# Optimization experiments

Measured on AMD Instinct MI355X. Metric: run time of the kernel, lower is better.

## Reference

```python
import jax, jax.numpy as jnp
import numpy as np

B_, CIN, HH, WW = 2, 64, 64, 64
D_MODEL, D_INNER, D_STATE, DT_RANK, D_CONV = 64, 128, 16, 32, 3


def setup_inputs() -> dict:
    key = jax.random.key(0)
    ks = jax.random.split(key, 16)
    w = lambda k, shape: jax.random.normal(k, shape, jnp.float32) * 0.05
    # dt_proj bias init (torch: inv-softplus of dt sampled in [dt_min, dt_max])
    dt = jnp.exp(jax.random.uniform(ks[10], (D_INNER,)) * (np.log(0.1) - np.log(0.001)) + np.log(0.001))
    dt = jnp.clip(dt, 1e-4, None)
    inv_dt = dt + jnp.log(-jnp.expm1(-dt))
    A = jnp.tile(jnp.arange(1, D_STATE + 1, dtype=jnp.float32), (D_INNER, 1))
    return {
        "rgb_feat": jax.random.normal(ks[0], (B_, CIN, HH, WW), jnp.float32),
        "dte_feat": jax.random.normal(ks[1], (B_, CIN, HH, WW), jnp.float32),
        "conv1_w": w(ks[2], (D_MODEL, CIN)), "conv1_b": jnp.zeros((D_MODEL,), jnp.float32),
        "conv2_w": w(ks[3], (D_MODEL, CIN)), "conv2_b": jnp.zeros((D_MODEL,), jnp.float32),
        "conv3_w": w(ks[4], (CIN, D_MODEL)), "conv3_b": jnp.zeros((CIN,), jnp.float32),
        "norm_w": jnp.ones((D_MODEL,), jnp.float32),
        "in_proj_w": w(ks[5], (2 * D_INNER, D_MODEL)),
        "conv1d_w": w(ks[6], (D_INNER, D_CONV)), "conv1d_b": jnp.zeros((D_INNER,), jnp.float32),
        "x_proj_w": w(ks[7], (DT_RANK + 2 * D_STATE, D_INNER)),
        "dt_proj_w": jax.random.uniform(ks[8], (D_INNER, DT_RANK), jnp.float32, -DT_RANK ** -0.5, DT_RANK ** -0.5),
        "dt_proj_b": inv_dt,
        "A_log": jnp.log(A),
        "Dp": jnp.ones((D_INNER,), jnp.float32),
        "out_proj_w": w(ks[9], (D_MODEL, D_INNER)),
    }


def _conv1x1(x, w, b):
    return jnp.einsum('bchw,oc->bohw', x, w) + b[None, :, None, None]


def _rmsnorm(x, w, eps=1e-5):
    return x * jax.lax.rsqrt(jnp.mean(x * x, axis=-1, keepdims=True) + eps) * w


def _dwconv1d(x, w, b):
    # x: [B,L,D]; depthwise conv, kernel 3, padding 1 (same length)
    xt = jnp.transpose(x, (0, 2, 1))  # [B,D,L]
    y = jax.lax.conv_general_dilated(xt, w[:, None, :], (1,), [(1, 1)],
                                     dimension_numbers=('NCH', 'OIH', 'NCH'),
                                     feature_group_count=D_INNER)
    return jnp.transpose(y + b[None, :, None], (0, 2, 1))


def _mamba(x, h, p):
    # x: [B,L,d_model]
    xz = x @ p['in_proj_w'].T                      # [B,L,2*d_inner]
    xc, z = jnp.split(xz, 2, axis=-1)
    xc = jax.nn.silu(_dwconv1d(xc, p['conv1d_w'], p['conv1d_b']))
    A = -jnp.exp(p['A_log'])                       # [D,S]
    dbc = xc @ p['x_proj_w'].T                     # [B,L,dt_rank+2S]
    delta, Bm, Cm = jnp.split(dbc, [DT_RANK, DT_RANK + D_STATE], axis=-1)
    delta = jax.nn.softplus(delta @ p['dt_proj_w'].T + p['dt_proj_b'])  # [B,L,D]
    deltaA = jnp.exp(delta[..., None] * A)         # [B,L,D,S]
    BX = delta[..., None] * Bm[:, :, None, :] * xc[..., None]  # [B,L,D,S]
    h = deltaA * h + BX
    y = jnp.einsum('blds,bls->bld', h, Cm) + p['Dp'] * xc
    out = (y * jax.nn.silu(z)) @ p['out_proj_w'].T
    return out, h


def _residual_block(x4d, h, p):
    B, C, H, W = x4d.shape
    x = jnp.transpose(x4d.reshape(B, C, H * W), (0, 2, 1))  # [B,L,C]
    x = _rmsnorm(x, p['norm_w'])
    out, h = _mamba(x, h, p)
    out = out + x
    return jnp.transpose(out, (0, 2, 1)).reshape(B, C, H, W), h


def _rsfm(rgb_feat, dte_feat, conv1_w, conv1_b, conv2_w, conv2_b, conv3_w, conv3_b,
          norm_w, in_proj_w, conv1d_w, conv1d_b, x_proj_w, dt_proj_w, dt_proj_b,
          A_log, Dp, out_proj_w):
    p = dict(norm_w=norm_w, in_proj_w=in_proj_w, conv1d_w=conv1d_w, conv1d_b=conv1d_b,
             x_proj_w=x_proj_w, dt_proj_w=dt_proj_w, dt_proj_b=dt_proj_b,
             A_log=A_log, Dp=Dp, out_proj_w=out_proj_w)
    rgb = _conv1x1(rgb_feat, conv1_w, conv1_b)
    dte = _conv1x1(dte_feat, conv2_w, conv2_b)
    B = rgb.shape[0]
    h = jnp.zeros((B, HH * WW, D_INNER, D_STATE), jnp.float32)
    out1, h = _residual_block(rgb, h, p)
    out2, h = _residual_block(dte + out1, h, p)
    out3, h = _residual_block(rgb + out2, h, p)
    out4, h = _residual_block(dte + out3, h, p)
    out5, h = _residual_block(rgb + out4, h, p)
    out6, h = _residual_block(dte + out5, h, p)
    return _conv1x1(out6, conv3_w, conv3_b), h


def reference(rgb_feat, dte_feat, conv1_w, conv1_b, conv2_w, conv2_b, conv3_w, conv3_b,
              norm_w, in_proj_w, conv1d_w, conv1d_b, x_proj_w, dt_proj_w, dt_proj_b,
              A_log, Dp, out_proj_w):
    return _rsfm(rgb_feat, dte_feat, conv1_w, conv1_b, conv2_w, conv2_b, conv3_w, conv3_b,
                 norm_w, in_proj_w, conv1d_w, conv1d_b, x_proj_w, dt_proj_w, dt_proj_b,
                 A_log, Dp, out_proj_w)
```

## Files before the change

### kernel.cpp

```cpp
#include <hip/hip_runtime.h>

typedef unsigned short u16;
typedef unsigned int u32;

#define LSEQ 4096
#define NPOS 8192

__device__ __forceinline__ float bf2f(u16 u){
  union { u32 i; float f; } v; v.i = ((u32)u) << 16; return v.f;
}
__device__ __forceinline__ u16 f2bf(float f){
  union { float f; u32 i; } v; v.f = f;
  u32 x = v.i;
  return (u16)((x + 0x7fffu + ((x >> 16) & 1u)) >> 16);
}
__device__ __forceinline__ float2 up2(u32 u){
  union { u32 i; float f; } a, b;
  a.i = u << 16; b.i = u & 0xffff0000u;
  float2 r; r.x = a.f; r.y = b.f; return r;
}
__device__ __forceinline__ u32 pk2(float a, float b){
  return (u32)f2bf(a) | ((u32)f2bf(b) << 16);
}
__device__ __forceinline__ float silu_f(float x){ return x / (1.f + __expf(-x)); }
__device__ __forceinline__ float softplus_f(float x){
  return fmaxf(x, 0.f) + log1pf(__expf(-fabsf(x)));
}

__global__ __launch_bounds__(256) void k_prep(
    const float* __restrict__ ipw, const float* __restrict__ xpw,
    const float* __restrict__ dtw, const float* __restrict__ opw,
    const float* __restrict__ w1, const float* __restrict__ w2,
    const float* __restrict__ w3, const float* __restrict__ alog,
    float* __restrict__ ipT, float* __restrict__ xpT,
    float* __restrict__ dtT, float* __restrict__ opT,
    float* __restrict__ w1T, float* __restrict__ w2T,
    float* __restrict__ w3T, float* __restrict__ Aneg)
{
  int t = blockIdx.x * 256 + threadIdx.x;
  if (t < 16384){ int o = t >> 6, c = t & 63; ipT[c * 256 + o] = ipw[t]; }
  if (t < 8192){ int o = t >> 7, d = t & 127; xpT[d * 64 + o] = xpw[t]; }
  if (t < 4096){ int d = t >> 5, r = t & 31; dtT[r * 128 + d] = dtw[t]; }
  if (t < 8192){ int o = t >> 7, d = t & 127; opT[d * 64 + o] = opw[t]; }
  if (t < 4096){ int o = t >> 6, c = t & 63;
                 w1T[c*64+o] = w1[t]; w2T[c*64+o] = w2[t]; w3T[c*64+o] = w3[t]; }
  if (t < 2048){ Aneg[t] = -__expf(alog[t]); }
}

__global__ __launch_bounds__(256) void k_convin(
    const float* __restrict__ rgb, const float* __restrict__ dte,
    const float* __restrict__ w1T, const float* __restrict__ b1,
    const float* __restrict__ w2T, const float* __restrict__ b2,
    float* __restrict__ rgbp, float* __restrict__ dtep)
{
  __shared__ __align__(16) float xt[64][64];
  __shared__ __align__(16) float ot[64][65];
  const int tid = threadIdx.x;
  const int which = blockIdx.x & 1;
  const int n0 = (blockIdx.x >> 1) * 64;
  const int b = n0 >> 12, l0 = n0 & 4095;
  const float* src = which ? dte : rgb;
  const float* wT  = which ? w2T : w1T;
  const float* bb  = which ? b2 : b1;
  float* o = which ? dtep : rgbp;

  #pragma unroll
  for (int j = 0; j < 16; j++){
    int idx = tid + 256 * j;
    int c = idx >> 6, p = idx & 63;
    xt[c][p] = src[(size_t)b * 262144 + (size_t)c * 4096 + l0 + p];
  }
  __syncthreads();

  const int pos = tid & 63;
  const int cb  = (tid >> 6) * 16;
  float acc[16];
  #pragma unroll
  for (int j = 0; j < 16; j++) acc[j] = bb[cb + j];
  for (int c = 0; c < 64; c++){
    float xv = xt[c][pos];
    #pragma unroll
    for (int j = 0; j < 16; j++) acc[j] += wT[c*64 + cb + j] * xv;
  }
  #pragma unroll
  for (int j = 0; j < 16; j++) ot[pos][cb + j] = acc[j];
  __syncthreads();
  #pragma unroll
  for (int j = 0; j < 16; j++){
    int idx = tid + 256 * j;
    int p = idx >> 6, c = idx & 63;
    o[(size_t)(n0 + p)*64 + c] = ot[p][c];
  }
}

__global__ __launch_bounds__(256) void k_pre(
    const float* __restrict__ xin, const float* __restrict__ normw,
    const float* __restrict__ ipT,
    float* __restrict__ xn, float* __restrict__ xcp, float* __restrict__ zs)
{
  __shared__ __align__(16) float xnl[4][2][64];
  const int wv = threadIdx.x >> 6, lane = threadIdx.x & 63;
  const int n0 = (blockIdx.x * 4 + wv) * 2;
  float nw = normw[lane];
  #pragma unroll
  for (int p = 0; p < 2; p++){
    int n = n0 + p;
    float v = xin[(size_t)n*64 + lane];
    float ss = v * v;
    for (int m = 32; m > 0; m >>= 1) ss += __shfl_xor(ss, m);
    v = v * rsqrtf(ss * (1.f/64.f) + 1e-5f) * nw;
    xn[(size_t)n*64 + lane] = v;
    xnl[wv][p][lane] = v;
  }
  float ac[2][4] = {};
  for (int c = 0; c < 64; c++){
    float w0 = ipT[c*256 + lane],       w1 = ipT[c*256 + 64 + lane];
    float w2 = ipT[c*256 + 128 + lane], w3 = ipT[c*256 + 192 + lane];
    #pragma unroll
    for (int p = 0; p < 2; p++){
      float xv = xnl[wv][p][c];
      ac[p][0] += w0*xv; ac[p][1] += w1*xv; ac[p][2] += w2*xv; ac[p][3] += w3*xv;
    }
  }
  #pragma unroll
  for (int p = 0; p < 2; p++){
    int n = n0 + p;
    xcp[(size_t)n*128 + lane]      = ac[p][0];
    xcp[(size_t)n*128 + 64 + lane] = ac[p][1];
    zs[(size_t)n*128 + lane]       = silu_f(ac[p][2]);
    zs[(size_t)n*128 + 64 + lane]  = silu_f(ac[p][3]);
  }
}

__global__ __launch_bounds__(256) void k_step(
    const float* __restrict__ xcpA, float* __restrict__ xcpB,
    float* __restrict__ zs, float* __restrict__ xn,
    u16* __restrict__ hbf, float* __restrict__ hfin,
    const float* __restrict__ base_next,
    const float* __restrict__ xpT, const float* __restrict__ dtT,
    const float* __restrict__ opT, const float* __restrict__ Aneg,
    const float* __restrict__ c1w, const float* __restrict__ c1b,
    const float* __restrict__ dtb, const float* __restrict__ Dpw,
    const float* __restrict__ normw, const float* __restrict__ ipT,
    int hasH, int fusePre)
{
  __shared__ __align__(16) float xcl[4][2][128];
  __shared__ __align__(16) float dbl[4][2][64];
  __shared__ __align__(16) float yzl[4][2][128];
  __shared__ __align__(16) float xnl[4][2][64];
  const int wv = threadIdx.x >> 6, lane = threadIdx.x & 63;
  const int n0 = (blockIdx.x * 4 + wv) * 2;
  const int d0 = lane, d1 = 64 + lane;

  float cw00 = c1w[d0*3+0], cw01 = c1w[d0*3+1], cw02 = c1w[d0*3+2];
  float cw10 = c1w[d1*3+0], cw11 = c1w[d1*3+1], cw12 = c1w[d1*3+2];
  float cb0 = c1b[d0], cb1 = c1b[d1];

  float xc0[2], xc1[2];
  #pragma unroll
  for (int p = 0; p < 2; p++){
    int n = n0 + p, l = n & 4095;
    const float* xr = xcpA + (size_t)n * 128;
    float am0 = 0.f, am1 = 0.f, ap0 = 0.f, ap1 = 0.f;
    if (l > 0)    { am0 = xr[d0 - 128]; am1 = xr[d1 - 128]; }
    float a00 = xr[d0], a01 = xr[d1];
    if (l < 4095) { ap0 = xr[d0 + 128]; ap1 = xr[d1 + 128]; }
    float v0 = silu_f(cw00*am0 + cw01*a00 + cw02*ap0 + cb0);
    float v1 = silu_f(cw10*am1 + cw11*a01 + cw12*ap1 + cb1);
    xc0[p] = v0; xc1[p] = v1;
    xcl[wv][p][d0] = v0; xcl[wv][p][d1] = v1;
  }

  {
    float xa[2] = {0,0};
    for (int d = 0; d < 128; d++){
      float w = xpT[d*64 + lane];
      #pragma unroll
      for (int p = 0; p < 2; p++) xa[p] += w * xcl[wv][p][d];
    }
    #pragma unroll
    for (int p = 0; p < 2; p++) dbl[wv][p][lane] = xa[p];
  }

  float dl0[2], dl1[2];
  {
    float tb0 = dtb[d0], tb1 = dtb[d1];
    float da0[2] = {tb0, tb0}, da1[2] = {tb1, tb1};
    for (int r = 0; r < 32; r++){
      float w0 = dtT[r*128 + d0], w1 = dtT[r*128 + d1];
      #pragma unroll
      for (int p = 0; p < 2; p++){
        float bv = dbl[wv][p][r];
        da0[p] += w0 * bv; da1[p] += w1 * bv;
      }
    }
    #pragma unroll
    for (int p = 0; p < 2; p++){ dl0[p] = softplus_f(da0[p]); dl1[p] = softplus_f(da1[p]); }
  }

  float an0[16], an1[16];
  {
    const float4* A0 = (const float4*)(Aneg + d0*16);
    const float4* A1 = (const float4*)(Aneg + d1*16);
    #pragma unroll
    for (int q = 0; q < 4; q++){
      float4 a = A0[q]; an0[q*4+0]=a.x; an0[q*4+1]=a.y; an0[q*4+2]=a.z; an0[q*4+3]=a.w;
      float4 b = A1[q]; an1[q*4+0]=b.x; an1[q*4+1]=b.y; an1[q*4+2]=b.z; an1[q*4+3]=b.w;
    }
  }
  float dp0 = Dpw[d0], dp1 = Dpw[d1];

  #pragma unroll 1
  for (int p = 0; p < 2; p++){
    int n = n0 + p;
    float Bm[16], Cm[16];
    {
      const float4* bb = (const float4*)&dbl[wv][p][32];
      const float4* cc = (const float4*)&dbl[wv][p][48];
      #pragma unroll
      for (int q = 0; q < 4; q++){
        float4 a = bb[q]; Bm[q*4+0]=a.x; Bm[q*4+1]=a.y; Bm[q*4+2]=a.z; Bm[q*4+3]=a.w;
        float4 b = cc[q]; Cm[q*4+0]=b.x; Cm[q*4+1]=b.y; Cm[q*4+2]=b.z; Cm[q*4+3]=b.w;
      }
    }
    u16* hp0 = hbf + ((size_t)n*2048 + (size_t)d0*16);
    u16* hp1 = hbf + ((size_t)n*2048 + (size_t)d1*16);
    float h0[16], h1[16];
    if (hasH){
      #pragma unroll
      for (int q = 0; q < 2; q++){
        uint4 v = ((const uint4*)hp0)[q];
        float2 t0=up2(v.x), t1=up2(v.y), t2=up2(v.z), t3=up2(v.w);
        h0[q*8+0]=t0.x; h0[q*8+1]=t0.y; h0[q*8+2]=t1.x; h0[q*8+3]=t1.y;
        h0[q*8+4]=t2.x; h0[q*8+5]=t2.y; h0[q*8+6]=t3.x; h0[q*8+7]=t3.y;
        uint4 w = ((const uint4*)hp1)[q];
        float2 s0=up2(w.x), s1=up2(w.y), s2=up2(w.z), s3=up2(w.w);
        h1[q*8+0]=s0.x; h1[q*8+1]=s0.y; h1[q*8+2]=s1.x; h1[q*8+3]=s1.y;
        h1[q*8+4]=s2.x; h1[q*8+5]=s2.y; h1[q*8+6]=s3.x; h1[q*8+7]=s3.y;
      }
    } else {
      #pragma unroll
      for (int s = 0; s < 16; s++){ h0[s]=0.f; h1[s]=0.f; }
    }
    float y0 = 0.f, y1 = 0.f;
    float bx0 = dl0[p] * xc0[p], bx1 = dl1[p] * xc1[p];
    #pragma unroll
    for (int s = 0; s < 16; s++){
      h0[s] = __expf(dl0[p]*an0[s])*h0[s] + bx0*Bm[s];
      y0 = fmaf(h0[s], Cm[s], y0);
      h1[s] = __expf(dl1[p]*an1[s])*h1[s] + bx1*Bm[s];
      y1 = fmaf(h1[s], Cm[s], y1);
    }
    if (fusePre){
      #pragma unroll
      for (int q = 0; q < 2; q++){
        uint4 v;
        v.x = pk2(h0[q*8+0], h0[q*8+1]); v.y = pk2(h0[q*8+2], h0[q*8+3]);
        v.z = pk2(h0[q*8+4], h0[q*8+5]); v.w = pk2(h0[q*8+6], h0[q*8+7]);
        ((uint4*)hp0)[q] = v;
        uint4 w;
        w.x = pk2(h1[q*8+0], h1[q*8+1]); w.y = pk2(h1[q*8+2], h1[q*8+3]);
        w.z = pk2(h1[q*8+4], h1[q*8+5]); w.w = pk2(h1[q*8+6], h1[q*8+7]);
        ((uint4*)hp1)[q] = w;
      }
    } else {
      float4* f0 = (float4*)(hfin + (size_t)n*2048 + (size_t)d0*16);
      float4* f1 = (float4*)(hfin + (size_t)n*2048 + (size_t)d1*16);
      #pragma unroll
      for (int q = 0; q < 4; q++){
        float4 v; v.x=h0[q*4+0]; v.y=h0[q*4+1]; v.z=h0[q*4+2]; v.w=h0[q*4+3];
        f0[q] = v;
        float4 w; w.x=h1[q*4+0]; w.y=h1[q*4+1]; w.z=h1[q*4+2]; w.w=h1[q*4+3];
        f1[q] = w;
      }
    }
    y0 += dp0 * xc0[p];
    y1 += dp1 * xc1[p];
    yzl[wv][p][d0] = y0 * zs[(size_t)n*128 + d0];
    yzl[wv][p][d1] = y1 * zs[(size_t)n*128 + d1];
  }

  float oa[2] = {0,0};
  for (int d = 0; d < 128; d++){
    float w = opT[d*64 + lane];
    #pragma unroll
    for (int p = 0; p < 2; p++) oa[p] += w * yzl[wv][p][d];
  }

  float nw = normw[lane];
  if (fusePre){
    #pragma unroll
    for (int p = 0; p < 2; p++){
      int n = n0 + p;
      float v = oa[p] + xn[(size_t)n*64 + lane] + base_next[(size_t)n*64 + lane];
      float ss = v * v;
      for (int m = 32; m > 0; m >>= 1) ss += __shfl_xor(ss, m);
      v = v * rsqrtf(ss * (1.f/64.f) + 1e-5f) * nw;
      xn[(size_t)n*64 + lane] = v;
      xnl[wv][p][lane] = v;
    }
    float ac[2][4] = {};
    for (int c = 0; c < 64; c++){
      float w0 = ipT[c*256 + lane],       w1 = ipT[c*256 + 64 + lane];
      float w2 = ipT[c*256 + 128 + lane], w3 = ipT[c*256 + 192 + lane];
      #pragma unroll
      for (int p = 0; p < 2; p++){
        float xv = xnl[wv][p][c];
        ac[p][0] += w0*xv; ac[p][1] += w1*xv; ac[p][2] += w2*xv; ac[p][3] += w3*xv;
      }
    }
    #pragma unroll
    for (int p = 0; p < 2; p++){
      int n = n0 + p;
      xcpB[(size_t)n*128 + lane]      = ac[p][0];
      xcpB[(size_t)n*128 + 64 + lane] = ac[p][1];
      zs[(size_t)n*128 + lane]        = silu_f(ac[p][2]);
      zs[(size_t)n*128 + 64 + lane]   = silu_f(ac[p][3]);
    }
  } else {
    #pragma unroll
    for (int p = 0; p < 2; p++){
      int n = n0 + p;
      xcpB[(size_t)n*64 + lane] = oa[p] + xn[(size_t)n*64 + lane];
    }
  }
}

__global__ __launch_bounds__(256) void k_conv3(
    const float* __restrict__ out6, const float* __restrict__ w3T,
    const float* __restrict__ b3, float* __restrict__ out)
{
  __shared__ __align__(16) float t[64][65];
  const int tid = threadIdx.x;
  const int n0 = blockIdx.x * 64;
  #pragma unroll
  for (int i = 0; i < 16; i++){
    int idx = tid + 256*i;
    int r = idx >> 6, c = idx & 63;
    t[r][c] = out6[(size_t)(n0 + r)*64 + c];
  }
  __syncthreads();
  const int i = tid & 63;
  const int cb = (tid >> 6) * 16;
  float acc[16];
  #pragma unroll
  for (int j = 0; j < 16; j++) acc[j] = b3[cb + j];
  for (int o = 0; o < 64; o++){
    float xv = t[i][o];
    #pragma unroll
    for (int j = 0; j < 16; j++) acc[j] += w3T[o*64 + cb + j] * xv;
  }
  const int b = n0 >> 12;
  const int l = (n0 & 4095) + i;
  #pragma unroll
  for (int j = 0; j < 16; j++)
    out[(size_t)b*262144 + (size_t)(cb + j)*4096 + l] = acc[j];
}

extern "C" void kernel_launch(void* const* d_in, const int* in_sizes, int n_in,
                              void* d_out, int out_size, void* d_ws, size_t ws_size,
                              hipStream_t stream)
{
  const float* rgb  = (const float*)d_in[0];
  const float* dte  = (const float*)d_in[1];
  const float* w1   = (const float*)d_in[2];
  const float* b1   = (const float*)d_in[3];
  const float* w2   = (const float*)d_in[4];
  const float* b2   = (const float*)d_in[5];
  const float* w3   = (const float*)d_in[6];
  const float* b3   = (const float*)d_in[7];
  const float* nrm  = (const float*)d_in[8];
  const float* ipw  = (const float*)d_in[9];
  const float* c1w  = (const float*)d_in[10];
  const float* c1b  = (const float*)d_in[11];
  const float* xpw  = (const float*)d_in[12];
  const float* dtw  = (const float*)d_in[13];
  const float* dtb  = (const float*)d_in[14];
  const float* alog = (const float*)d_in[15];
  const float* Dpw  = (const float*)d_in[16];
  const float* opw  = (const float*)d_in[17];

  float* outc = (float*)d_out;
  float* hfin = outc + 524288;

  float* ws   = (float*)d_ws;
  float* xcp0 = ws;
  float* xcp1 = ws + 1048576;
  float* rgbp = ws + 2097152;
  float* dtep = ws + 2621440;
  float* xnb  = ws + 3145728;
  float* zsb  = ws + 3670016;
  float* wb   = ws + 4718592;
  float* ipT  = wb;
  float* xpT  = wb + 16384;
  float* dtT  = wb + 24576;
  float* opT  = wb + 28672;
  float* w1T  = wb + 36864;
  float* w2T  = wb + 40960;
  float* w3T  = wb + 45056;
  float* Aneg = wb + 49152;
  u16*   hbf  = (u16*)(ws + 4769792);

  k_prep<<<64, 256, 0, stream>>>(ipw, xpw, dtw, opw, w1, w2, w3, alog,
                                 ipT, xpT, dtT, opT, w1T, w2T, w3T, Aneg);
  k_convin<<<256, 256, 0, stream>>>(rgb, dte, w1T, b1, w2T, b2, rgbp, dtep);
  k_pre<<<1024, 256, 0, stream>>>(rgbp, nrm, ipT, xnb, xcp0, zsb);

  float* xa[2] = {xcp0, xcp1};
  for (int k = 0; k < 6; k++){
    const float* base = (k == 5) ? rgbp  : ((k & 1) ? rgbp : dtep);
    k_step<<<1024, 256, 0, stream>>>(xa[k & 1], xa[(k & 1) ^ 1], zsb, xnb,
                                     hbf, hfin, base,
                                     xpT, dtT, opT, Aneg, c1w, c1b, dtb, Dpw,
                                     nrm, ipT, (k > 0) ? 1 : 0, (k < 5) ? 1 : 0);
  }
  k_conv3<<<128, 256, 0, stream>>>(xcp0, w3T, b3, outc);
}
```

Baseline: 369.5 us.

## Fuse all residual blocks into one kernel with halo-recompute tiles

Replaces the chain of conv-in, pre, six step kernels and conv-out with a single kernel. Each block handles 32 positions plus an 8-position halo on each side, and recomputes the halo so the depthwise conv stays local across all six blocks. The bf16 SSM state lives in registers and activations stay in shared memory, which removes the per-step global round trips of state and activations. The cost is redundant halo compute (48 positions computed per 32 output), higher register and LDS pressure, and only 256 blocks to fill the GPU.

```diff
diff --git a/kernel.cpp b/kernel.cpp
--- a/kernel.cpp
+++ b/kernel.cpp
@@ -3,21 +3,15 @@
 typedef unsigned short u16;
 typedef unsigned int u32;
 
-#define LSEQ 4096
-#define NPOS 8192
-
-__device__ __forceinline__ float bf2f(u16 u){
-  union { u32 i; float f; } v; v.i = ((u32)u) << 16; return v.f;
+__device__ __forceinline__ float2 up2(u32 u){
+  union { u32 i; float f; } a, b;
+  a.i = u << 16; b.i = u & 0xffff0000u;
+  float2 r; r.x = a.f; r.y = b.f; return r;
 }
 __device__ __forceinline__ u16 f2bf(float f){
   union { float f; u32 i; } v; v.f = f;
   u32 x = v.i;
   return (u16)((x + 0x7fffu + ((x >> 16) & 1u)) >> 16);
-}
-__device__ __forceinline__ float2 up2(u32 u){
-  union { u32 i; float f; } a, b;
-  a.i = u << 16; b.i = u & 0xffff0000u;
-  float2 r; r.x = a.f; r.y = b.f; return r;
 }
 __device__ __forceinline__ u32 pk2(float a, float b){
   return (u32)f2bf(a) | ((u32)f2bf(b) << 16);
@@ -47,314 +41,300 @@
   if (t < 2048){ Aneg[t] = -__expf(alog[t]); }
 }
 
-__global__ __launch_bounds__(256) void k_convin(
+#define CPB 48
+#define PPW 6
+
+__global__ __launch_bounds__(512, 2) void k_fused(
     const float* __restrict__ rgb, const float* __restrict__ dte,
     const float* __restrict__ w1T, const float* __restrict__ b1,
     const float* __restrict__ w2T, const float* __restrict__ b2,
-    float* __restrict__ rgbp, float* __restrict__ dtep)
-{
-  __shared__ __align__(16) float xt[64][64];
-  __shared__ __align__(16) float ot[64][65];
-  const int tid = threadIdx.x;
-  const int which = blockIdx.x & 1;
-  const int n0 = (blockIdx.x >> 1) * 64;
-  const int b = n0 >> 12, l0 = n0 & 4095;
-  const float* src = which ? dte : rgb;
-  const float* wT  = which ? w2T : w1T;
-  const float* bb  = which ? b2 : b1;
-  float* o = which ? dtep : rgbp;
-
-  #pragma unroll
-  for (int j = 0; j < 16; j++){
-    int idx = tid + 256 * j;
-    int c = idx >> 6, p = idx & 63;
-    xt[c][p] = src[(size_t)b * 262144 + (size_t)c * 4096 + l0 + p];
-  }
-  __syncthreads();
-
-  const int pos = tid & 63;
-  const int cb  = (tid >> 6) * 16;
-  float acc[16];
-  #pragma unroll
-  for (int j = 0; j < 16; j++) acc[j] = bb[cb + j];
-  for (int c = 0; c < 64; c++){
-    float xv = xt[c][pos];
-    #pragma unroll
-    for (int j = 0; j < 16; j++) acc[j] += wT[c*64 + cb + j] * xv;
-  }
-  #pragma unroll
-  for (int j = 0; j < 16; j++) ot[pos][cb + j] = acc[j];
-  __syncthreads();
-  #pragma unroll
-  for (int j = 0; j < 16; j++){
-    int idx = tid + 256 * j;
-    int p = idx >> 6, c = idx & 63;
-    o[(size_t)(n0 + p)*64 + c] = ot[p][c];
-  }
-}
-
-__global__ __launch_bounds__(256) void k_pre(
-    const float* __restrict__ xin, const float* __restrict__ normw,
-    const float* __restrict__ ipT,
-    float* __restrict__ xn, float* __restrict__ xcp, float* __restrict__ zs)
-{
-  __shared__ __align__(16) float xnl[4][2][64];
-  const int wv = threadIdx.x >> 6, lane = threadIdx.x & 63;
-  const int n0 = (blockIdx.x * 4 + wv) * 2;
-  float nw = normw[lane];
-  #pragma unroll
-  for (int p = 0; p < 2; p++){
-    int n = n0 + p;
-    float v = xin[(size_t)n*64 + lane];
-    float ss = v * v;
-    for (int m = 32; m > 0; m >>= 1) ss += __shfl_xor(ss, m);
-    v = v * rsqrtf(ss * (1.f/64.f) + 1e-5f) * nw;
-    xn[(size_t)n*64 + lane] = v;
-    xnl[wv][p][lane] = v;
-  }
-  float ac[2][4] = {};
-  for (int c = 0; c < 64; c++){
-    float w0 = ipT[c*256 + lane],       w1 = ipT[c*256 + 64 + lane];
-    float w2 = ipT[c*256 + 128 + lane], w3 = ipT[c*256 + 192 + lane];
-    #pragma unroll
-    for (int p = 0; p < 2; p++){
-      float xv = xnl[wv][p][c];
-      ac[p][0] += w0*xv; ac[p][1] += w1*xv; ac[p][2] += w2*xv; ac[p][3] += w3*xv;
-    }
-  }
-  #pragma unroll
-  for (int p = 0; p < 2; p++){
-    int n = n0 + p;
-    xcp[(size_t)n*128 + lane]      = ac[p][0];
-    xcp[(size_t)n*128 + 64 + lane] = ac[p][1];
-    zs[(size_t)n*128 + lane]       = silu_f(ac[p][2]);
-    zs[(size_t)n*128 + 64 + lane]  = silu_f(ac[p][3]);
-  }
-}
-
-__global__ __launch_bounds__(256) void k_step(
-    const float* __restrict__ xcpA, float* __restrict__ xcpB,
-    float* __restrict__ zs, float* __restrict__ xn,
-    u16* __restrict__ hbf, float* __restrict__ hfin,
-    const float* __restrict__ base_next,
+    const float* __restrict__ w3T, const float* __restrict__ b3,
+    const float* __restrict__ normw, const float* __restrict__ ipT,
     const float* __restrict__ xpT, const float* __restrict__ dtT,
     const float* __restrict__ opT, const float* __restrict__ Aneg,
     const float* __restrict__ c1w, const float* __restrict__ c1b,
     const float* __restrict__ dtb, const float* __restrict__ Dpw,
-    const float* __restrict__ normw, const float* __restrict__ ipT,
-    int hasH, int fusePre)
+    float* __restrict__ outc, float* __restrict__ hfin)
 {
-  __shared__ __align__(16) float xcl[4][2][128];
-  __shared__ __align__(16) float dbl[4][2][64];
-  __shared__ __align__(16) float yzl[4][2][128];
-  __shared__ __align__(16) float xnl[4][2][64];
-  const int wv = threadIdx.x >> 6, lane = threadIdx.x & 63;
-  const int n0 = (blockIdx.x * 4 + wv) * 2;
+  __shared__ __align__(16) float xcp[CPB][128];
+  __shared__ __align__(16) float xcs[CPB][128];
+  __shared__ __align__(16) float dblS[CPB][64];
+  __shared__ __align__(16) float xns[CPB][64];
+  __shared__ __align__(16) float bA[CPB][64];
+  __shared__ __align__(16) float bB[CPB][64];
+  __shared__ __align__(16) float ansS[16][129];
+  __shared__ __align__(16) float xpW[8192];
+  __shared__ __align__(16) float dtW[4096];
+
+  const int tid = threadIdx.x;
+  const int wv = tid >> 6, lane = tid & 63;
+  const int b = blockIdx.x;
+  const int batch = b >> 7;
+  const int lbase = ((b & 127) << 5) - 8;
+  const int cpw = wv * PPW;
   const int d0 = lane, d1 = 64 + lane;
 
-  float cw00 = c1w[d0*3+0], cw01 = c1w[d0*3+1], cw02 = c1w[d0*3+2];
-  float cw10 = c1w[d1*3+0], cw11 = c1w[d1*3+1], cw12 = c1w[d1*3+2];
-  float cb0 = c1b[d0], cb1 = c1b[d1];
-
-  float xc0[2], xc1[2];
+  for (int i = tid; i < 8192; i += 512) xpW[i] = xpT[i];
+  for (int i = tid; i < 4096; i += 512) dtW[i] = dtT[i];
+  for (int i = tid; i < 2048; i += 512) ansS[i & 15][i >> 4] = Aneg[i];
+
+  const float cw00 = c1w[d0*3+0], cw01 = c1w[d0*3+1], cw02 = c1w[d0*3+2];
+  const float cw10 = c1w[d1*3+0], cw11 = c1w[d1*3+1], cw12 = c1w[d1*3+2];
+  const float cb0 = c1b[d0], cb1 = c1b[d1];
+  const float tb0 = dtb[d0], tb1 = dtb[d1];
+  const float dp0 = Dpw[d0], dp1 = Dpw[d1];
+  const float nw = normw[lane];
+
+  int lp[PPW];
   #pragma unroll
-  for (int p = 0; p < 2; p++){
-    int n = n0 + p, l = n & 4095;
-    const float* xr = xcpA + (size_t)n * 128;
-    float am0 = 0.f, am1 = 0.f, ap0 = 0.f, ap1 = 0.f;
-    if (l > 0)    { am0 = xr[d0 - 128]; am1 = xr[d1 - 128]; }
-    float a00 = xr[d0], a01 = xr[d1];
-    if (l < 4095) { ap0 = xr[d0 + 128]; ap1 = xr[d1 + 128]; }
-    float v0 = silu_f(cw00*am0 + cw01*a00 + cw02*ap0 + cb0);
-    float v1 = silu_f(cw10*am1 + cw11*a01 + cw12*ap1 + cb1);
-    xc0[p] = v0; xc1[p] = v1;
-    xcl[wv][p][d0] = v0; xcl[wv][p][d1] = v1;
+  for (int p = 0; p < PPW; p++) lp[p] = lbase + cpw + p;
+
+  {
+    const float* rp = rgb + (size_t)batch * 262144;
+    const float* dq_ = dte + (size_t)batch * 262144;
+    int lc[PPW];
+    #pragma unroll
+    for (int p = 0; p < PPW; p++) lc[p] = min(max(lp[p], 0), 4095);
+    float accA[PPW], accB[PPW];
+    float bb1 = b1[lane], bb2 = b2[lane];
+    #pragma unroll
+    for (int p = 0; p < PPW; p++){ accA[p] = bb1; accB[p] = bb2; }
+    #pragma unroll 4
+    for (int c = 0; c < 64; c++){
+      float wA = w1T[c*64 + lane], wB = w2T[c*64 + lane];
+      const float* rc = rp + c*4096;
+      const float* dc = dq_ + c*4096;
+      #pragma unroll
+      for (int p = 0; p < PPW; p++){
+        accA[p] = fmaf(wA, rc[lc[p]], accA[p]);
+        accB[p] = fmaf(wB, dc[lc[p]], accB[p]);
+      }
+    }
+    #pragma unroll
+    for (int p = 0; p < PPW; p++){ bA[cpw+p][lane] = accA[p]; bB[cpw+p][lane] = accB[p]; }
   }
 
+  float xnr[PPW], zs0[PPW], zs1[PPW];
   {
-    float xa[2] = {0,0};
-    for (int d = 0; d < 128; d++){
-      float w = xpT[d*64 + lane];
-      #pragma unroll
-      for (int p = 0; p < 2; p++) xa[p] += w * xcl[wv][p][d];
-    }
-    #pragma unroll
-    for (int p = 0; p < 2; p++) dbl[wv][p][lane] = xa[p];
-  }
-
-  float dl0[2], dl1[2];
-  {
-    float tb0 = dtb[d0], tb1 = dtb[d1];
-    float da0[2] = {tb0, tb0}, da1[2] = {tb1, tb1};
-    for (int r = 0; r < 32; r++){
-      float w0 = dtT[r*128 + d0], w1 = dtT[r*128 + d1];
-      #pragma unroll
-      for (int p = 0; p < 2; p++){
-        float bv = dbl[wv][p][r];
-        da0[p] += w0 * bv; da1[p] += w1 * bv;
-      }
-    }
-    #pragma unroll
-    for (int p = 0; p < 2; p++){ dl0[p] = softplus_f(da0[p]); dl1[p] = softplus_f(da1[p]); }
-  }
-
-  float an0[16], an1[16];
-  {
-    const float4* A0 = (const float4*)(Aneg + d0*16);
-    const float4* A1 = (const float4*)(Aneg + d1*16);
-    #pragma unroll
-    for (int q = 0; q < 4; q++){
-      float4 a = A0[q]; an0[q*4+0]=a.x; an0[q*4+1]=a.y; an0[q*4+2]=a.z; an0[q*4+3]=a.w;
-      float4 b = A1[q]; an1[q*4+0]=b.x; an1[q*4+1]=b.y; an1[q*4+2]=b.z; an1[q*4+3]=b.w;
-    }
-  }
-  float dp0 = Dpw[d0], dp1 = Dpw[d1];
-
-  #pragma unroll 1
-  for (int p = 0; p < 2; p++){
-    int n = n0 + p;
-    float Bm[16], Cm[16];
-    {
-      const float4* bb = (const float4*)&dbl[wv][p][32];
-      const float4* cc = (const float4*)&dbl[wv][p][48];
-      #pragma unroll
-      for (int q = 0; q < 4; q++){
-        float4 a = bb[q]; Bm[q*4+0]=a.x; Bm[q*4+1]=a.y; Bm[q*4+2]=a.z; Bm[q*4+3]=a.w;
-        float4 b = cc[q]; Cm[q*4+0]=b.x; Cm[q*4+1]=b.y; Cm[q*4+2]=b.z; Cm[q*4+3]=b.w;
-      }
-    }
-    u16* hp0 = hbf + ((size_t)n*2048 + (size_t)d0*16);
-    u16* hp1 = hbf + ((size_t)n*2048 + (size_t)d1*16);
-    float h0[16], h1[16];
-    if (hasH){
-      #pragma unroll
-      for (int q = 0; q < 2; q++){
-        uint4 v = ((const uint4*)hp0)[q];
-        float2 t0=up2(v.x), t1=up2(v.y), t2=up2(v.z), t3=up2(v.w);
-        h0[q*8+0]=t0.x; h0[q*8+1]=t0.y; h0[q*8+2]=t1.x; h0[q*8+3]=t1.y;
-        h0[q*8+4]=t2.x; h0[q*8+5]=t2.y; h0[q*8+6]=t3.x; h0[q*8+7]=t3.y;
-        uint4 w = ((const uint4*)hp1)[q];
-        float2 s0=up2(w.x), s1=up2(w.y), s2=up2(w.z), s3=up2(w.w);
-        h1[q*8+0]=s0.x; h1[q*8+1]=s0.y; h1[q*8+2]=s1.x; h1[q*8+3]=s1.y;
-        h1[q*8+4]=s2.x; h1[q*8+5]=s2.y; h1[q*8+6]=s3.x; h1[q*8+7]=s3.y;
-      }
-    } else {
-      #pragma unroll
-      for (int s = 0; s < 16; s++){ h0[s]=0.f; h1[s]=0.f; }
-    }
-    float y0 = 0.f, y1 = 0.f;
-    float bx0 = dl0[p] * xc0[p], bx1 = dl1[p] * xc1[p];
-    #pragma unroll
-    for (int s = 0; s < 16; s++){
-      h0[s] = __expf(dl0[p]*an0[s])*h0[s] + bx0*Bm[s];
-      y0 = fmaf(h0[s], Cm[s], y0);
-      h1[s] = __expf(dl1[p]*an1[s])*h1[s] + bx1*Bm[s];
-      y1 = fmaf(h1[s], Cm[s], y1);
-    }
-    if (fusePre){
-      #pragma unroll
-      for (int q = 0; q < 2; q++){
-        uint4 v;
-        v.x = pk2(h0[q*8+0], h0[q*8+1]); v.y = pk2(h0[q*8+2], h0[q*8+3]);
-        v.z = pk2(h0[q*8+4], h0[q*8+5]); v.w = pk2(h0[q*8+6], h0[q*8+7]);
-        ((uint4*)hp0)[q] = v;
-        uint4 w;
-        w.x = pk2(h1[q*8+0], h1[q*8+1]); w.y = pk2(h1[q*8+2], h1[q*8+3]);
-        w.z = pk2(h1[q*8+4], h1[q*8+5]); w.w = pk2(h1[q*8+6], h1[q*8+7]);
-        ((uint4*)hp1)[q] = w;
-      }
-    } else {
-      float4* f0 = (float4*)(hfin + (size_t)n*2048 + (size_t)d0*16);
-      float4* f1 = (float4*)(hfin + (size_t)n*2048 + (size_t)d1*16);
-      #pragma unroll
-      for (int q = 0; q < 4; q++){
-        float4 v; v.x=h0[q*4+0]; v.y=h0[q*4+1]; v.z=h0[q*4+2]; v.w=h0[q*4+3];
-        f0[q] = v;
-        float4 w; w.x=h1[q*4+0]; w.y=h1[q*4+1]; w.z=h1[q*4+2]; w.w=h1[q*4+3];
-        f1[q] = w;
-      }
-    }
-    y0 += dp0 * xc0[p];
-    y1 += dp1 * xc1[p];
-    yzl[wv][p][d0] = y0 * zs[(size_t)n*128 + d0];
-    yzl[wv][p][d1] = y1 * zs[(size_t)n*128 + d1];
-  }
-
-  float oa[2] = {0,0};
-  for (int d = 0; d < 128; d++){
-    float w = opT[d*64 + lane];
-    #pragma unroll
-    for (int p = 0; p < 2; p++) oa[p] += w * yzl[wv][p][d];
-  }
-
-  float nw = normw[lane];
-  if (fusePre){
-    #pragma unroll
-    for (int p = 0; p < 2; p++){
-      int n = n0 + p;
-      float v = oa[p] + xn[(size_t)n*64 + lane] + base_next[(size_t)n*64 + lane];
+    #pragma unroll
+    for (int p = 0; p < PPW; p++){
+      float v = bA[cpw+p][lane];
       float ss = v * v;
       for (int m = 32; m > 0; m >>= 1) ss += __shfl_xor(ss, m);
       v = v * rsqrtf(ss * (1.f/64.f) + 1e-5f) * nw;
-      xn[(size_t)n*64 + lane] = v;
-      xnl[wv][p][lane] = v;
-    }
-    float ac[2][4] = {};
+      xnr[p] = v; xns[cpw+p][lane] = v;
+    }
+    float a0[PPW]={}, a1[PPW]={}, a2[PPW]={}, a3[PPW]={};
+    #pragma unroll 4
     for (int c = 0; c < 64; c++){
-      float w0 = ipT[c*256 + lane],       w1 = ipT[c*256 + 64 + lane];
-      float w2 = ipT[c*256 + 128 + lane], w3 = ipT[c*256 + 192 + lane];
-      #pragma unroll
-      for (int p = 0; p < 2; p++){
-        float xv = xnl[wv][p][c];
-        ac[p][0] += w0*xv; ac[p][1] += w1*xv; ac[p][2] += w2*xv; ac[p][3] += w3*xv;
-      }
-    }
-    #pragma unroll
-    for (int p = 0; p < 2; p++){
-      int n = n0 + p;
-      xcpB[(size_t)n*128 + lane]      = ac[p][0];
-      xcpB[(size_t)n*128 + 64 + lane] = ac[p][1];
-      zs[(size_t)n*128 + lane]        = silu_f(ac[p][2]);
-      zs[(size_t)n*128 + 64 + lane]   = silu_f(ac[p][3]);
-    }
-  } else {
-    #pragma unroll
-    for (int p = 0; p < 2; p++){
-      int n = n0 + p;
-      xcpB[(size_t)n*64 + lane] = oa[p] + xn[(size_t)n*64 + lane];
+      float w0 = ipT[c*256 + lane];
+      float w1 = ipT[c*256 + 64 + lane];
+      float w2 = ipT[c*256 + 128 + lane];
+      float w3 = ipT[c*256 + 192 + lane];
+      #pragma unroll
+      for (int p = 0; p < PPW; p++){
+        float xv = xns[cpw+p][c];
+        a0[p]=fmaf(w0,xv,a0[p]); a1[p]=fmaf(w1,xv,a1[p]);
+        a2[p]=fmaf(w2,xv,a2[p]); a3[p]=fmaf(w3,xv,a3[p]);
+      }
+    }
+    #pragma unroll
+    for (int p = 0; p < PPW; p++){
+      xcp[cpw+p][d0] = a0[p]; xcp[cpw+p][d1] = a1[p];
+      zs0[p] = silu_f(a2[p]); zs1[p] = silu_f(a3[p]);
     }
   }
-}
-
-__global__ __launch_bounds__(256) void k_conv3(
-    const float* __restrict__ out6, const float* __restrict__ w3T,
-    const float* __restrict__ b3, float* __restrict__ out)
-{
-  __shared__ __align__(16) float t[64][65];
-  const int tid = threadIdx.x;
-  const int n0 = blockIdx.x * 64;
-  #pragma unroll
-  for (int i = 0; i < 16; i++){
-    int idx = tid + 256*i;
-    int r = idx >> 6, c = idx & 63;
-    t[r][c] = out6[(size_t)(n0 + r)*64 + c];
+
+  u32 hp0[PPW][8] = {}, hp1[PPW][8] = {};
+
+  #pragma unroll 1
+  for (int k = 0; k < 6; k++){
+    __syncthreads();
+
+    float xc0[PPW], xc1[PPW];
+    #pragma unroll
+    for (int p = 0; p < PPW; p++){
+      int cp = cpw + p;
+      float am0=0.f, am1=0.f, ap0=0.f, ap1=0.f;
+      if (cp > 0 && lp[p] > 0)       { am0 = xcp[cp-1][d0]; am1 = xcp[cp-1][d1]; }
+      float a00 = xcp[cp][d0], a01 = xcp[cp][d1];
+      if (cp < CPB-1 && lp[p] < 4095){ ap0 = xcp[cp+1][d0]; ap1 = xcp[cp+1][d1]; }
+      float v0 = silu_f(fmaf(cw00,am0, fmaf(cw01,a00, fmaf(cw02,ap0, cb0))));
+      float v1 = silu_f(fmaf(cw10,am1, fmaf(cw11,a01, fmaf(cw12,ap1, cb1))));
+      xc0[p] = v0; xc1[p] = v1;
+      xcs[cp][d0] = v0; xcs[cp][d1] = v1;
+    }
+    __syncthreads();
+
+    {
+      float xa[PPW] = {};
+      #pragma unroll 2
+      for (int dq = 0; dq < 32; dq++){
+        float w0 = xpW[(dq*4+0)*64 + lane], w1 = xpW[(dq*4+1)*64 + lane];
+        float w2 = xpW[(dq*4+2)*64 + lane], w3 = xpW[(dq*4+3)*64 + lane];
+        #pragma unroll
+        for (int p = 0; p < PPW; p++){
+          float4 xv = *(const float4*)&xcs[cpw+p][dq*4];
+          xa[p] = fmaf(w0,xv.x, fmaf(w1,xv.y, fmaf(w2,xv.z, fmaf(w3,xv.w, xa[p]))));
+        }
+      }
+      #pragma unroll
+      for (int p = 0; p < PPW; p++) dblS[cpw+p][lane] = xa[p];
+    }
+
+    float dl0[PPW], dl1[PPW];
+    {
+      float da0[PPW], da1[PPW];
+      #pragma unroll
+      for (int p = 0; p < PPW; p++){ da0[p] = tb0; da1[p] = tb1; }
+      #pragma unroll 4
+      for (int r = 0; r < 32; r++){
+        float w0 = dtW[r*128 + d0], w1 = dtW[r*128 + d1];
+        #pragma unroll
+        for (int p = 0; p < PPW; p++){
+          float bv = dblS[cpw+p][r];
+          da0[p] = fmaf(w0, bv, da0[p]); da1[p] = fmaf(w1, bv, da1[p]);
+        }
+      }
+      #pragma unroll
+      for (int p = 0; p < PPW; p++){ dl0[p] = softplus_f(da0[p]); dl1[p] = softplus_f(da1[p]); }
+    }
+
+    float y0[PPW] = {}, y1[PPW] = {};
+    float bx0[PPW], bx1[PPW];
+    #pragma unroll
+    for (int p = 0; p < PPW; p++){ bx0[p] = dl0[p]*xc0[p]; bx1[p] = dl1[p]*xc1[p]; }
+    if (k < 5){
+      #pragma unroll
+      for (int q = 0; q < 8; q++){
+        float a0e = ansS[2*q][d0], a0o = ansS[2*q+1][d0];
+        float a1e = ansS[2*q][d1], a1o = ansS[2*q+1][d1];
+        #pragma unroll
+        for (int p = 0; p < PPW; p++){
+          int cp = cpw + p;
+          float2 Bv = *(const float2*)&dblS[cp][32 + 2*q];
+          float2 Cv = *(const float2*)&dblS[cp][48 + 2*q];
+          float2 h0 = up2(hp0[p][q]);
+          float2 h1 = up2(hp1[p][q]);
+          float n0e = fmaf(__expf(dl0[p]*a0e), h0.x, bx0[p]*Bv.x);
+          float n0o = fmaf(__expf(dl0[p]*a0o), h0.y, bx0[p]*Bv.y);
+          float n1e = fmaf(__expf(dl1[p]*a1e), h1.x, bx1[p]*Bv.x);
+          float n1o = fmaf(__expf(dl1[p]*a1o), h1.y, bx1[p]*Bv.y);
+          y0[p] = fmaf(n0e, Cv.x, y0[p]); y0[p] = fmaf(n0o, Cv.y, y0[p]);
+          y1[p] = fmaf(n1e, Cv.x, y1[p]); y1[p] = fmaf(n1o, Cv.y, y1[p]);
+          hp0[p][q] = pk2(n0e, n0o);
+          hp1[p][q] = pk2(n1e, n1o);
+        }
+      }
+    } else {
+      #pragma unroll
+      for (int q = 0; q < 8; q++){
+        float a0e = ansS[2*q][d0], a0o = ansS[2*q+1][d0];
+        float a1e = ansS[2*q][d1], a1o = ansS[2*q+1][d1];
+        #pragma unroll
+        for (int p = 0; p < PPW; p++){
+          int cp = cpw + p;
+          float2 Bv = *(const float2*)&dblS[cp][32 + 2*q];
+          float2 Cv = *(const float2*)&dblS[cp][48 + 2*q];
+          float2 h0 = up2(hp0[p][q]);
+          float2 h1 = up2(hp1[p][q]);
+          float n0e = fmaf(__expf(dl0[p]*a0e), h0.x, bx0[p]*Bv.x);
+          float n0o = fmaf(__expf(dl0[p]*a0o), h0.y, bx0[p]*Bv.y);
+          float n1e = fmaf(__expf(dl1[p]*a1e), h1.x, bx1[p]*Bv.x);
+          float n1o = fmaf(__expf(dl1[p]*a1o), h1.y, bx1[p]*Bv.y);
+          y0[p] = fmaf(n0e, Cv.x, y0[p]); y0[p] = fmaf(n0o, Cv.y, y0[p]);
+          y1[p] = fmaf(n1e, Cv.x, y1[p]); y1[p] = fmaf(n1o, Cv.y, y1[p]);
+          if (cp >= 8 && cp < 40){
+            size_t nI = (size_t)b*32 + (size_t)(cp - 8);
+            float2 s0; s0.x = n0e; s0.y = n0o;
+            float2 s1; s1.x = n1e; s1.y = n1o;
+            *(float2*)(hfin + nI*2048 + (size_t)d0*16 + 2*q) = s0;
+            *(float2*)(hfin + nI*2048 + (size_t)d1*16 + 2*q) = s1;
+          }
+        }
+      }
+    }
+
+    #pragma unroll
+    for (int p = 0; p < PPW; p++){
+      int cp = cpw + p;
+      float yy0 = fmaf(dp0, xc0[p], y0[p]);
+      float yy1 = fmaf(dp1, xc1[p], y1[p]);
+      xcs[cp][d0] = yy0 * zs0[p];
+      xcs[cp][d1] = yy1 * zs1[p];
+    }
+
+    float oa[PPW] = {};
+    #pragma unroll 2
+    for (int dq = 0; dq < 32; dq++){
+      float w0 = opT[(dq*4+0)*64 + lane], w1 = opT[(dq*4+1)*64 + lane];
+      float w2 = opT[(dq*4+2)*64 + lane], w3 = opT[(dq*4+3)*64 + lane];
+      #pragma unroll
+      for (int p = 0; p < PPW; p++){
+        float4 yv = *(const float4*)&xcs[cpw+p][dq*4];
+        oa[p] = fmaf(w0,yv.x, fmaf(w1,yv.y, fmaf(w2,yv.z, fmaf(w3,yv.w, oa[p]))));
+      }
+    }
+
+    if (k < 5){
+      const float (*bs_)[64] = (k & 1) ? bA : bB;
+      #pragma unroll
+      for (int p = 0; p < PPW; p++){
+        int cp = cpw + p;
+        float v = oa[p] + xnr[p] + bs_[cp][lane];
+        float ss = v * v;
+        for (int m = 32; m > 0; m >>= 1) ss += __shfl_xor(ss, m);
+        v = v * rsqrtf(ss * (1.f/64.f) + 1e-5f) * nw;
+        xnr[p] = v; xns[cp][lane] = v;
+      }
+      float a0[PPW]={}, a1[PPW]={}, a2[PPW]={}, a3[PPW]={};
+      #pragma unroll 4
+      for (int c = 0; c < 64; c++){
+        float w0 = ipT[c*256 + lane];
+        float w1 = ipT[c*256 + 64 + lane];
+        float w2 = ipT[c*256 + 128 + lane];
+        float w3 = ipT[c*256 + 192 + lane];
+        #pragma unroll
+        for (int p = 0; p < PPW; p++){
+          float xv = xns[cpw+p][c];
+          a0[p]=fmaf(w0,xv,a0[p]); a1[p]=fmaf(w1,xv,a1[p]);
+          a2[p]=fmaf(w2,xv,a2[p]); a3[p]=fmaf(w3,xv,a3[p]);
+        }
+      }
+      #pragma unroll
+      for (int p = 0; p < PPW; p++){
+        int cp = cpw + p;
+        xcp[cp][d0] = a0[p]; xcp[cp][d1] = a1[p];
+        zs0[p] = silu_f(a2[p]); zs1[p] = silu_f(a3[p]);
+      }
+    } else {
+      #pragma unroll
+      for (int p = 0; p < PPW; p++) dblS[cpw+p][lane] = oa[p] + xnr[p];
+    }
   }
-  __syncthreads();
-  const int i = tid & 63;
-  const int cb = (tid >> 6) * 16;
-  float acc[16];
-  #pragma unroll
-  for (int j = 0; j < 16; j++) acc[j] = b3[cb + j];
-  for (int o = 0; o < 64; o++){
-    float xv = t[i][o];
-    #pragma unroll
-    for (int j = 0; j < 16; j++) acc[j] += w3T[o*64 + cb + j] * xv;
+
+  {
+    float o3[PPW];
+    float bb3 = b3[lane];
+    #pragma unroll
+    for (int p = 0; p < PPW; p++) o3[p] = bb3;
+    #pragma unroll 2
+    for (int cq = 0; cq < 16; cq++){
+      float w0 = w3T[(cq*4+0)*64 + lane], w1 = w3T[(cq*4+1)*64 + lane];
+      float w2 = w3T[(cq*4+2)*64 + lane], w3v = w3T[(cq*4+3)*64 + lane];
+      #pragma unroll
+      for (int p = 0; p < PPW; p++){
+        float4 vv = *(const float4*)&dblS[cpw+p][cq*4];
+        o3[p] = fmaf(w0,vv.x, fmaf(w1,vv.y, fmaf(w2,vv.z, fmaf(w3v,vv.w, o3[p]))));
+      }
+    }
+    #pragma unroll
+    for (int p = 0; p < PPW; p++){
+      int cp = cpw + p;
+      if (cp >= 8 && cp < 40)
+        outc[(size_t)batch*262144 + (size_t)lane*4096 + lp[p]] = o3[p];
+    }
   }
-  const int b = n0 >> 12;
-  const int l = (n0 & 4095) + i;
-  #pragma unroll
-  for (int j = 0; j < 16; j++)
-    out[(size_t)b*262144 + (size_t)(cb + j)*4096 + l] = acc[j];
 }
 
 extern "C" void kernel_launch(void* const* d_in, const int* in_sizes, int n_in,
@@ -383,14 +363,7 @@
   float* outc = (float*)d_out;
   float* hfin = outc + 524288;
 
-  float* ws   = (float*)d_ws;
-  float* xcp0 = ws;
-  float* xcp1 = ws + 1048576;
-  float* rgbp = ws + 2097152;
-  float* dtep = ws + 2621440;
-  float* xnb  = ws + 3145728;
-  float* zsb  = ws + 3670016;
-  float* wb   = ws + 4718592;
+  float* wb   = (float*)d_ws;
   float* ipT  = wb;
   float* xpT  = wb + 16384;
   float* dtT  = wb + 24576;
@@ -399,20 +372,10 @@
   float* w2T  = wb + 40960;
   float* w3T  = wb + 45056;
   float* Aneg = wb + 49152;
-  u16*   hbf  = (u16*)(ws + 4769792);
 
   k_prep<<<64, 256, 0, stream>>>(ipw, xpw, dtw, opw, w1, w2, w3, alog,
                                  ipT, xpT, dtT, opT, w1T, w2T, w3T, Aneg);
-  k_convin<<<256, 256, 0, stream>>>(rgb, dte, w1T, b1, w2T, b2, rgbp, dtep);
-  k_pre<<<1024, 256, 0, stream>>>(rgbp, nrm, ipT, xnb, xcp0, zsb);
-
-  float* xa[2] = {xcp0, xcp1};
-  for (int k = 0; k < 6; k++){
-    const float* base = (k == 5) ? rgbp  : ((k & 1) ? rgbp : dtep);
-    k_step<<<1024, 256, 0, stream>>>(xa[k & 1], xa[(k & 1) ^ 1], zsb, xnb,
-                                     hbf, hfin, base,
-                                     xpT, dtT, opT, Aneg, c1w, c1b, dtb, Dpw,
-                                     nrm, ipT, (k > 0) ? 1 : 0, (k < 5) ? 1 : 0);
-  }
-  k_conv3<<<128, 256, 0, stream>>>(xcp0, w3T, b3, outc);
-}
+  k_fused<<<256, 512, 0, stream>>>(rgb, dte, w1T, b1, w2T, b2, w3T, b3,
+                                   nrm, ipT, xpT, dtT, opT, Aneg,
+                                   c1w, c1b, dtb, Dpw, outc, hfin);
+}
```

Result: slower. 627.1 us (+69.7%).
